# Optimization experiments

Measured on AMD Instinct MI355X. Metric: run time of the kernel, lower is better.

The kernel has to match this reference:

```python
import jax, jax.numpy as jnp
import numpy as np

B_IMG, T_PER, DIN = 8, 4096, 1176
D, E, BN, L, TOP_K, OUT = 1024, 8, 64, 4, 2, 4096


def setup_inputs() -> dict:
    key = jax.random.key(0)
    ks = jax.random.split(key, 16)
    s = 0.02
    inp = {
        "pixel_values": jax.random.normal(ks[0], (B_IMG * T_PER, DIN), jnp.float32),
        "image_grid_thw": jnp.tile(jnp.array([[1, 64, 64]], dtype=jnp.int64), (B_IMG, 1)),
        # in_proj (no bias)
        "w_in": jax.random.normal(ks[1], (DIN, D), jnp.float32) * s,
        # skin classifier: Linear(D,64) -> ReLU -> Linear(64,3)
        "w_sc1": jax.random.normal(ks[2], (D, 64), jnp.float32) * s,
        "b_sc1": jnp.zeros((64,), jnp.float32),
        "w_sc2": jax.random.normal(ks[3], (64, 3), jnp.float32) * s,
        "b_sc2": jnp.zeros((3,), jnp.float32),
        # per-adapter-layer routers (stacked over L)
        "w_rimg": jax.random.normal(ks[4], (L, D, E), jnp.float32) * s,
        "w_rskin": jax.random.normal(ks[5], (L, 3, E), jnp.float32) * s,
        # per-layer, per-expert MLP: Linear(D,BN) -> ReLU -> Linear(BN,D)
        "ew1": jax.random.normal(ks[6], (L, E, D, BN), jnp.float32) * s,
        "eb1": jnp.zeros((L, E, BN), jnp.float32),
        "ew2": jax.random.normal(ks[7], (L, E, BN, D), jnp.float32) * s,
        "eb2": jnp.zeros((L, E, D), jnp.float32),
        # out_proj
        "w_out": jax.random.normal(ks[8], (D, OUT), jnp.float32) * s,
        "b_out": jnp.zeros((OUT,), jnp.float32),
    }
    return inp


def _forward(pixel_values, image_grid_thw, w_in, w_sc1, b_sc1, w_sc2, b_sc2,
             w_rimg, w_rskin, ew1, eb1, ew2, eb2, w_out, b_out):
    B = image_grid_thw.shape[0]
    T = pixel_values.shape[0] // B  # equal chunk sizes (t*h*w identical per image)
    x = pixel_values.reshape(B, T, -1)

    def per_image(xc):  # xc: [T, din]
        h = xc @ w_in  # [T, D]
        g = h.mean(0)
        skin_logits = jax.nn.relu(g @ w_sc1 + b_sc1) @ w_sc2 + b_sc2  # [3]
        skin_probs = jax.nn.softmax(skin_logits)

        def layer(carry, params):
            h, aux = carry
            wri, wrs, W1, B1, W2, B2 = params
            logits = h @ wri + skin_probs @ wrs  # [T, E]
            probs = jax.nn.softmax(logits, axis=-1)
            tp, ti = jax.lax.top_k(probs, TOP_K)
            tp = tp / (tp.sum(-1, keepdims=True) + 1e-6)
            rows = jnp.arange(h.shape[0])[:, None]
            # dense per-token expert weights (0 for non-selected experts)
            wfull = jnp.zeros_like(probs).at[rows, ti].add(tp)
            mask = jnp.zeros_like(probs).at[rows, ti].add(1.0)
            h1 = jax.nn.relu(jnp.einsum('td,edb->teb', h, W1) + B1)  # [T,E,BN]
            h2 = jnp.einsum('teb,ebd->ted', h1, W2) + B2             # [T,E,D]
            moe_out = jnp.einsum('ted,te->td', h2, wfull)
            aux = aux + (probs.mean(0) * mask.mean(0)).sum() * probs.shape[-1]
            return (h + moe_out, aux), None

        (h, aux), _ = jax.lax.scan(layer, (h, jnp.zeros((), h.dtype)),
                                   (w_rimg, w_rskin, ew1, eb1, ew2, eb2))
        return h.mean(0), skin_logits, aux

    pooled, skin_logits, aux = jax.vmap(per_image)(x)
    vision_proj = pooled @ w_out + b_out
    return pooled, vision_proj, aux.sum(), skin_logits


def reference(pixel_values, image_grid_thw, w_in, w_sc1, b_sc1, w_sc2, b_sc2,
              w_rimg, w_rskin, ew1, eb1, ew2, eb2, w_out, b_out):
    return _forward(pixel_values, image_grid_thw, w_in, w_sc1, b_sc1, w_sc2, b_sc2,
                    w_rimg, w_rskin, ew1, eb1, ew2, eb2, w_out, b_out)
```

## Files before the change

kernel.cpp:

```cpp
#include <hip/hip_runtime.h>
#include <math.h>

#define TPI  4096
#define TT   32768
#define DIN  1176
#define KP   1216
#define DM   1024
#define NE   8
#define BN   64
#define NL   4
#define DOUT 4096
#define TBLK 32

typedef __attribute__((ext_vector_type(4))) float floatx4;
typedef __attribute__((ext_vector_type(8))) short bf16x8;
typedef unsigned int uint;

__device__ inline short f2bf(float x) {
    unsigned u = __float_as_uint(x);
    u += 0x7fffu + ((u >> 16) & 1u);
    return (short)(u >> 16);
}
__device__ inline float bf2f(short h) {
    return __uint_as_float(((unsigned)(unsigned short)h) << 16);
}

#define GLP(p) ((const __attribute__((address_space(1))) void*)(p))
#define LDSP(p) ((__attribute__((address_space(3))) void*)(p))
#define ASYNC16(g, s) __builtin_amdgcn_global_load_lds(GLP(g), LDSP(s), 16, 0, 0)

#define OFF_H0    0ul
#define OFF_H1    67108864ul
#define OFF_XB    67108864ul
#define OFF_WBT   146800640ul
#define OFF_E1T   149291008ul
#define OFF_E2T   153485312ul
#define OFF_BTOK  157679616ul
#define OFF_BW1   157810688ul
#define OFF_BW2   157941760ul
#define OFF_T2E   158072832ul
#define OFF_T2W   158203904ul
#define OFF_Z     158466048ul
#define Z_BYTES   39232ul
#define OFF_RB    158505280ul
#define OFF_WRT   158506304ul

__global__ __launch_bounds__(256) void convx_kernel(
    const float* __restrict__ X, short* __restrict__ Xb)
{
    const long row = blockIdx.x;
    const float* src = X + row * (long)DIN;
    short* dst = Xb + row * (long)KP;
    for (int i = threadIdx.x; i < 304; i += 256) {
        short4 s;
        if (i < 294) {
            float4 v = *(const float4*)(src + i * 4);
            s.x = f2bf(v.x); s.y = f2bf(v.y); s.z = f2bf(v.z); s.w = f2bf(v.w);
        } else {
            s.x = 0; s.y = 0; s.z = 0; s.w = 0;
        }
        *(short4*)(dst + i * 4) = s;
    }
}

__global__ __launch_bounds__(256) void transp_kernel(
    const float* __restrict__ src, short* __restrict__ dst, int RS, int CS, int DK)
{
    __shared__ float tb[64][65];
    const int kt = blockIdx.x * 64, nt = blockIdx.y * 64;
    const long sb = (long)blockIdx.z * RS * CS;
    const long db = (long)blockIdx.z * CS * DK;
    const int rr = threadIdx.x >> 6, cc = threadIdx.x & 63;
#pragma unroll
    for (int i = 0; i < 16; ++i) {
        int r = i * 4 + rr;
        int k = kt + r, n = nt + cc;
        tb[r][cc] = (k < RS && n < CS) ? src[sb + (long)k * CS + n] : 0.0f;
    }
    __syncthreads();
#pragma unroll
    for (int i = 0; i < 16; ++i) {
        int r = i * 4 + rr;
        int n = nt + r, k = kt + cc;
        if (n < CS && k < DK) dst[db + (long)n * DK + k] = f2bf(tb[cc][r]);
    }
}

__global__ __launch_bounds__(256) void wrt_kernel(
    const float* __restrict__ w_rimg, short* __restrict__ wrT)
{
    const int l = blockIdx.x >> 4, e = blockIdx.x & 15;
    short* dst = wrT + ((long)l * 16 + e) * 1024;
    if (e < 8) {
        const float* src = w_rimg + (long)l * 8192 + e;
        for (int k = threadIdx.x; k < 1024; k += 256) dst[k] = f2bf(src[k * 8]);
    } else {
        for (int k = threadIdx.x; k < 1024; k += 256) dst[k] = 0;
    }
}

__global__ __launch_bounds__(256) void gemm_in_mfma(
    const short* __restrict__ Xb, const short* __restrict__ Wbt,
    short* __restrict__ Hb, float* __restrict__ g)
{
    __shared__ __align__(16) short As[128 * 64];
    __shared__ __align__(16) short Bs[128 * 64];
    const int tid = threadIdx.x;
    const int m0 = blockIdx.x * 128, n0 = blockIdx.y * 128;
    const int w = tid >> 6, lane = tid & 63;
    const int quad = lane >> 4, l15 = lane & 15;
    const int wm = (w >> 1) * 64, wn = (w & 1) * 64;

    floatx4 acc[4][4];
#pragma unroll
    for (int i = 0; i < 4; ++i)
#pragma unroll
        for (int j = 0; j < 4; ++j) acc[i][j] = 0.0f;

    const int r = tid >> 3;
    const int gofs = ((tid & 7) ^ (r & 7)) * 8;
    const short* ap = Xb + (long)(m0 + r) * KP + gofs;
    const short* bp = Wbt + (long)(n0 + r) * KP + gofs;
    short* asd = As + tid * 8;
    short* bsd = Bs + tid * 8;
    const int rx = l15 & 7;

    for (int k0 = 0; k0 < KP; k0 += 64) {
        __syncthreads();
#pragma unroll
        for (int i = 0; i < 4; ++i) {
            ASYNC16(ap + (long)i * 32 * KP + k0, asd + i * 2048);
            ASYNC16(bp + (long)i * 32 * KP + k0, bsd + i * 2048);
        }
        __syncthreads();
#pragma unroll
        for (int kk = 0; kk < 2; ++kk) {
            bf16x8 af[4], bfr[4];
#pragma unroll
            for (int i = 0; i < 4; ++i)
                af[i] = *(const bf16x8*)&As[(wm + i * 16 + l15) * 64 + (((kk * 4 + quad)) ^ rx) * 8];
#pragma unroll
            for (int j = 0; j < 4; ++j)
                bfr[j] = *(const bf16x8*)&Bs[(wn + j * 16 + l15) * 64 + (((kk * 4 + quad)) ^ rx) * 8];
#pragma unroll
            for (int i = 0; i < 4; ++i)
#pragma unroll
                for (int j = 0; j < 4; ++j)
                    acc[i][j] = __builtin_amdgcn_mfma_f32_16x16x32_bf16(af[i], bfr[j], acc[i][j], 0, 0, 0);
        }
    }
    const int img = m0 >> 12;
#pragma unroll
    for (int j = 0; j < 4; ++j) {
        float cs = 0.0f;
#pragma unroll
        for (int i = 0; i < 4; ++i)
#pragma unroll
            for (int r2 = 0; r2 < 4; ++r2) {
                short hv = f2bf(acc[i][j][r2]);
                Hb[(long)(m0 + wm + i * 16 + quad * 4 + r2) * DM + n0 + wn + j * 16 + l15] =
                    hv;
                cs += bf2f(hv);
            }
        cs += __shfl_xor(cs, 16);
        cs += __shfl_xor(cs, 32);
        if (quad == 0)
            atomicAdd(&g[img * DM + n0 + wn + j * 16 + l15], cs * (1.0f / 4096.0f));
    }
}

__global__ __launch_bounds__(256) void colmean_kernel(
    const short* __restrict__ Hb, float* __restrict__ outp)
{
    const int col = blockIdx.x * 256 + threadIdx.x;
    const int img = blockIdx.y;
    const int t0 = blockIdx.z * 256;
    const short* p = Hb + ((long)img * TPI + t0) * DM + col;
    float s = 0.0f;
#pragma unroll 8
    for (int t = 0; t < 256; ++t) s += bf2f(p[(long)t * DM]);
    atomicAdd(&outp[img * DM + col], s * (1.0f / 4096.0f));
}

__global__ __launch_bounds__(256) void skin1_kernel(
    const float* __restrict__ g, const float* __restrict__ w_sc1,
    const float* __restrict__ b_sc1, float* __restrict__ hsg)
{
    __shared__ float red[4][64];
    const int img = blockIdx.x;
    const int part = threadIdx.x >> 6, c = threadIdx.x & 63;
    float s = 0.0f;
    for (int i = 0; i < 256; ++i) {
        int d = part * 256 + i;
        s += g[img * DM + d] * w_sc1[d * 64 + c];
    }
    red[part][c] = s;
    __syncthreads();
    if (part == 0) {
        float v = red[0][c] + red[1][c] + red[2][c] + red[3][c] + b_sc1[c];
        hsg[img * 64 + c] = fmaxf(v, 0.0f);
    }
}

__global__ __launch_bounds__(256) void skin2_kernel(
    const float* __restrict__ hsg, const float* __restrict__ w_sc2, const float* __restrict__ b_sc2,
    const float* __restrict__ w_rskin, float* __restrict__ skin_logits_out, float* __restrict__ rb)
{
    __shared__ float l3[24];
    __shared__ float sp[24];
    const int tid = threadIdx.x;
    if (tid < 24) {
        int img = tid / 3, j = tid % 3;
        float s = b_sc2[j];
        for (int c = 0; c < 64; ++c) s += hsg[img * 64 + c] * w_sc2[c * 3 + j];
        l3[tid] = s;
        skin_logits_out[tid] = s;
    }
    __syncthreads();
    if (tid < 8) {
        float v0 = l3[tid * 3], v1 = l3[tid * 3 + 1], v2 = l3[tid * 3 + 2];
        float m = fmaxf(v0, fmaxf(v1, v2));
        float e0 = expf(v0 - m), e1 = expf(v1 - m), e2 = expf(v2 - m);
        float inv = 1.0f / (e0 + e1 + e2);
        sp[tid * 3] = e0 * inv; sp[tid * 3 + 1] = e1 * inv; sp[tid * 3 + 2] = e2 * inv;
    }
    __syncthreads();
    {
        int l = tid >> 6, img = (tid >> 3) & 7, e = tid & 7;
        float s = 0.0f;
#pragma unroll
        for (int c = 0; c < 3; ++c) s += sp[img * 3 + c] * w_rskin[(l * 3 + c) * 8 + e];
        rb[tid] = s;
    }
}

__global__ __launch_bounds__(256) void router_kernel(
    const short* __restrict__ Hb, const short* __restrict__ wrT, const float* __restrict__ rb,
    uint* __restrict__ top2e, float* __restrict__ top2w, int* __restrict__ counts_pair,
    float* __restrict__ sum_probs, float* __restrict__ mask_cnt, int l)
{
    __shared__ __align__(16) short As[8 * 64 * 32];
    __shared__ float lgS[64 * 9];
    const int tid = threadIdx.x;
    const int tok0 = blockIdx.x * 64;
    const int img = tok0 >> 12;
    const int w = tid >> 6, lane = tid & 63;
    const int quad = lane >> 4, l15 = lane & 15;

    const short* rowptr = Hb + (long)(tok0 + w * 16 + (lane >> 2)) * DM + (lane & 3) * 8;
    short* sdst = As + tid * 8;
    const short* wrl = wrT + (long)l * 16 * 1024 + l15 * 1024 + quad * 8;

    floatx4 acc = 0.0f;
    for (int k0 = 0; k0 < DM; k0 += 256) {
        __syncthreads();
#pragma unroll
        for (int c = 0; c < 8; ++c) ASYNC16(rowptr + k0 + c * 32, sdst + c * 2048);
        __syncthreads();
#pragma unroll
        for (int c = 0; c < 8; ++c) {
            bf16x8 af = *(const bf16x8*)&As[c * 2048 + (w * 16 + l15) * 32 + quad * 8];
            bf16x8 bf = *(const bf16x8*)(wrl + k0 + c * 32);
            acc = __builtin_amdgcn_mfma_f32_16x16x32_bf16(af, bf, acc, 0, 0, 0);
        }
    }
    if (l15 < 8) {
#pragma unroll
        for (int r = 0; r < 4; ++r) lgS[(w * 16 + quad * 4 + r) * 9 + l15] = acc[r];
    }
    __syncthreads();

    if (tid < 64) {
        const int token = tok0 + tid;
        float p[8];
        float mx = -1e30f;
#pragma unroll
        for (int e = 0; e < 8; ++e) {
            float v = lgS[tid * 9 + e] + rb[l * 64 + img * 8 + e];
            p[e] = v; mx = fmaxf(mx, v);
        }
        float s = 0.0f;
#pragma unroll
        for (int e = 0; e < 8; ++e) { p[e] = expf(p[e] - mx); s += p[e]; }
        float inv = 1.0f / s;
#pragma unroll
        for (int e = 0; e < 8; ++e) p[e] *= inv;

        int i1 = 0; float b1v = p[0];
#pragma unroll
        for (int e = 1; e < 8; ++e) if (p[e] > b1v) { b1v = p[e]; i1 = e; }
        int i2 = -1; float b2v = -1.0f;
#pragma unroll
        for (int e = 0; e < 8; ++e) if (e != i1 && p[e] > b2v) { b2v = p[e]; i2 = e; }
        float den = b1v + b2v + 1e-6f;
        top2e[token] = (uint)i1 | ((uint)i2 << 8);
        top2w[2 * token] = b1v / den;
        top2w[2 * token + 1] = b2v / den;

        atomicAdd(&counts_pair[l * 64 + i1 * 8 + i2], 1);

        for (int slot = 0; slot < 2; ++slot) {
            int esel = slot ? i2 : i1;
#pragma unroll
            for (int e = 0; e < 8; ++e) {
                unsigned long long m = __ballot(esel == e);
                int pc = __popcll(m);
                if (pc && tid == (__ffsll(m) - 1))
                    atomicAdd(&mask_cnt[l * 64 + img * 8 + e], (float)pc);
            }
        }
#pragma unroll
        for (int e = 0; e < 8; ++e) {
            float rsum = p[e];
            for (int off = 32; off > 0; off >>= 1) rsum += __shfl_down(rsum, off);
            if (tid == 0) atomicAdd(&sum_probs[l * 64 + img * 8 + e], rsum);
        }
    }
}

__global__ __launch_bounds__(256) void scatter_kernel(
    const uint* __restrict__ top2e, const float* __restrict__ top2w,
    const int* __restrict__ counts_pair, int* __restrict__ cursors,
    int* __restrict__ btok, float* __restrict__ bw1, float* __restrict__ bw2, int l)
{
    __shared__ int pofS[64];
    const int tid = threadIdx.x;
    if (tid < 64) {
        int c = counts_pair[l * 64 + tid];
        int x = c;
#pragma unroll
        for (int off = 1; off < 64; off <<= 1) {
            int y = __shfl_up(x, off);
            if (tid >= off) x += y;
        }
        pofS[tid] = x - c;
    }
    __syncthreads();
    const int t = blockIdx.x * 256 + tid;
    const int lane = tid & 63;
    uint pe = top2e[t];
    int p = (int)(pe & 255u) * 8 + (int)((pe >> 8) & 255u);
    float w1 = top2w[2 * t], w2 = top2w[2 * t + 1];
    int myoff = pofS[p];
    unsigned long long rem = __ballot(true);
    while (rem) {
        int leader = __ffsll(rem) - 1;
        int pv = __shfl(p, leader);
        unsigned long long m = __ballot(p == pv);
        int basep = 0;
        if (lane == leader) basep = atomicAdd(&cursors[l * 64 + pv], __popcll(m));
        basep = __shfl(basep, leader);
        if (p == pv) {
            int pos = basep + __popcll(m & ((1ull << lane) - 1ull));
            int s = myoff + pos;
            btok[s] = t;
            bw1[s] = w1;
            bw2[s] = w2;
        }
        rem &= ~m;
    }
}

__global__ __launch_bounds__(256, 3) void expert_pair(
    const short* __restrict__ Hin, short* __restrict__ Hout,
    int* __restrict__ counts_pair,
    const int* __restrict__ btok, const float* __restrict__ bw1, const float* __restrict__ bw2,
    const short* __restrict__ ew1t, const float* __restrict__ eb1,
    const short* __restrict__ ew2t, const float* __restrict__ eb2,
    const short* __restrict__ wrT, const float* __restrict__ rb,
    uint* __restrict__ top2e, float* __restrict__ top2w,
    float* __restrict__ sum_probs, float* __restrict__ mask_cnt, int l)
{
    __shared__ __align__(16) short As[2][TBLK * 256];
    __shared__ __align__(16) short h1ab[2][TBLK * 72];
    __shared__ int tkS[TBLK];
    __shared__ float w1S[TBLK], w2S[TBLK];
    __shared__ int pofS[64], cntS[64], tpS[64];
    __shared__ int nworkS;
    __shared__ float spLDS[64], mkLDS[64];

    short* h1a = &h1ab[0][0];
    short* h1b = &h1ab[1][0];
    float* lgF = (float*)&h1ab[0][0];

    const int tid = threadIdx.x;
    const int w = tid >> 6, lane = tid & 63;
    const int quad = lane >> 4, l15 = lane & 15;

    if (tid < 64) {
        int c = counts_pair[l * 64 + tid];
        cntS[tid] = c;
        int x = c;
#pragma unroll
        for (int off = 1; off < 64; off <<= 1) {
            int y = __shfl_up(x, off);
            if (tid >= off) x += y;
        }
        pofS[tid] = x - c;
        int nb = (c + TBLK - 1) >> 5;
        int t = nb;
#pragma unroll
        for (int off = 1; off < 64; off <<= 1) {
            int y = __shfl_up(t, off);
            if (tid >= off) t += y;
        }
        tpS[tid] = t;
        if (tid == 63) nworkS = t;
    }
    __syncthreads();
    const int nwork = nworkS;

    const int bswz = (int)((blockIdx.x & 7) * (gridDim.x >> 3) + (blockIdx.x >> 3));

    const int srow0 = tid >> 5;
    const int sj = tid & 31;

    for (int wi = bswz; wi < nwork; wi += gridDim.x) {
        int p = 0;
        while (p < 63 && tpS[p] <= wi) ++p;
        const int cnt = cntS[p];
        const int nbp = (cnt + TBLK - 1) >> 5;
        const int base = (wi - (tpS[p] - nbp)) * TBLK;
        const int ea = p >> 3, eb = p & 7;
        const int off = pofS[p];
        const int lea = l * 8 + ea, leb = l * 8 + eb;

        __syncthreads();

        long srcrow[4];
#pragma unroll
        for (int cc = 0; cc < 4; ++cc) {
            const int row = cc * 8 + srow0;
            const int tokr = ((base + row) < cnt) ? btok[off + base + row] : 0;
            srcrow[cc] = (long)tokr * DM + ((sj ^ (row & 7)) << 3);
        }
        if (tid < TBLK) {
            bool valid = (base + tid) < cnt;
            int s = off + base + tid;
            tkS[tid] = valid ? btok[s] : 0;
            w1S[tid] = valid ? bw1[s] : 0.0f;
            w2S[tid] = valid ? bw2[s] : 0.0f;
        }
        if (tid < 64) { spLDS[tid] = 0.0f; mkLDS[tid] = 0.0f; }

#pragma unroll
        for (int cc = 0; cc < 4; ++cc)
            ASYNC16(Hin + srcrow[cc], &As[0][(cc * 256 + tid) * 8]);
        __syncthreads();

        floatx4 acc1a[2], acc1b[2];
#pragma unroll
        for (int i = 0; i < 2; ++i) { acc1a[i] = 0.0f; acc1b[i] = 0.0f; }
        const short* w1ap = ew1t + ((long)lea * BN + w * 16 + l15) * DM + quad * 8;
        const short* w1bp = ew1t + ((long)leb * BN + w * 16 + l15) * DM + quad * 8;

#pragma unroll
        for (int s = 0; s < 4; ++s) {
            const int nxt = (s < 3) ? (s + 1) * 256 : 0;
            short* dst = &As[(s & 1) ^ 1][0];
#pragma unroll
            for (int cc = 0; cc < 4; ++cc)
                ASYNC16(Hin + srcrow[cc] + nxt, dst + (cc * 256 + tid) * 8);
            const short* cur = &As[s & 1][0];
            const int k0 = s * 256;
#pragma unroll
            for (int c = 0; c < 8; ++c) {
                bf16x8 ba = *(const bf16x8*)(w1ap + k0 + c * 32);
                bf16x8 bb = *(const bf16x8*)(w1bp + k0 + c * 32);
#pragma unroll
                for (int i = 0; i < 2; ++i) {
                    const int tok = i * 16 + l15;
                    bf16x8 af = *(const bf16x8*)&cur[tok * 256 + (((c * 4 + quad) ^ (tok & 7)) << 3)];
                    acc1a[i] = __builtin_amdgcn_mfma_f32_16x16x32_bf16(af, ba, acc1a[i], 0, 0, 0);
                    acc1b[i] = __builtin_amdgcn_mfma_f32_16x16x32_bf16(af, bb, acc1b[i], 0, 0, 0);
                }
            }
            __syncthreads();
        }
        {
            float b1av = eb1[lea * BN + w * 16 + l15];
            float b1bv = eb1[leb * BN + w * 16 + l15];
#pragma unroll
            for (int i = 0; i < 2; ++i)
#pragma unroll
                for (int r = 0; r < 4; ++r) {
                    h1a[(i * 16 + quad * 4 + r) * 72 + w * 16 + l15] =
                        f2bf(fmaxf(acc1a[i][r] + b1av, 0.0f));
                    h1b[(i * 16 + quad * 4 + r) * 72 + w * 16 + l15] =
                        f2bf(fmaxf(acc1b[i][r] + b1bv, 0.0f));
                }
        }
        __syncthreads();

        bf16x8 hra[2][2], hrb[2][2];
#pragma unroll
        for (int kk = 0; kk < 2; ++kk)
#pragma unroll
            for (int tj = 0; tj < 2; ++tj) {
                hra[kk][tj] = *(const bf16x8*)&h1a[(tj * 16 + l15) * 72 + kk * 32 + quad * 8];
                hrb[kk][tj] = *(const bf16x8*)&h1b[(tj * 16 + l15) * 72 + kk * 32 + quad * 8];
            }

        const short* w2ap = ew2t + ((long)lea * DM + w * 16 + l15) * 64 + quad * 8;
        const short* w2bp = ew2t + ((long)leb * DM + w * 16 + l15) * 64 + quad * 8;
        const short* wrp = wrT + ((long)(l + 1 < NL ? l + 1 : 0) * 16 + l15) * 1024 + quad * 8;

        floatx4 acc_lg[2];
#pragma unroll
        for (int tf = 0; tf < 2; ++tf) acc_lg[tf] = 0.0f;

#pragma unroll
        for (int gidx = 0; gidx < 4; ++gidx) {
            const int g0 = gidx * 256;
            if (gidx < 3) {
                short* dst = &As[(gidx & 1) ^ 1][0];
#pragma unroll
                for (int cc = 0; cc < 4; ++cc)
                    ASYNC16(Hin + srcrow[cc] + (g0 + 256), dst + (cc * 256 + tid) * 8);
            }
            short* cur = &As[gidx & 1][0];
#pragma unroll
            for (int ns = 0; ns < 4; ++ns) {
                const int n0 = g0 + ns * 64;
                floatx4 a2a[2], a2b[2];
#pragma unroll
                for (int tj = 0; tj < 2; ++tj) { a2a[tj] = 0.0f; a2b[tj] = 0.0f; }
#pragma unroll
                for (int kk = 0; kk < 2; ++kk) {
                    bf16x8 wa = *(const bf16x8*)(w2ap + (long)n0 * 64 + kk * 32);
                    bf16x8 wb = *(const bf16x8*)(w2bp + (long)n0 * 64 + kk * 32);
#pragma unroll
                    for (int tj = 0; tj < 2; ++tj) {
                        a2a[tj] = __builtin_amdgcn_mfma_f32_16x16x32_bf16(wa, hra[kk][tj], a2a[tj], 0, 0, 0);
                        a2b[tj] = __builtin_amdgcn_mfma_f32_16x16x32_bf16(wb, hrb[kk][tj], a2b[tj], 0, 0, 0);
                    }
                }
                const int nloc = ns * 64 + w * 16 + quad * 4;
                const int jch = nloc >> 3, jof = nloc & 7;
                float4 b2av = *(const float4*)&eb2[lea * DM + g0 + nloc];
                float4 b2bv = *(const float4*)&eb2[leb * DM + g0 + nloc];
#pragma unroll
                for (int tj = 0; tj < 2; ++tj) {
                    int tk = tj * 16 + l15;
                    float w1v = w1S[tk], w2v = w2S[tk];
                    short* slot = &cur[tk * 256 + ((jch ^ (tk & 7)) << 3) + jof];
                    short4 res = *(short4*)slot;
                    short4 o;
                    o.x = f2bf(bf2f(res.x) + w1v * (a2a[tj][0] + b2av.x) + w2v * (a2b[tj][0] + b2bv.x));
                    o.y = f2bf(bf2f(res.y) + w1v * (a2a[tj][1] + b2av.y) + w2v * (a2b[tj][1] + b2bv.y));
                    o.z = f2bf(bf2f(res.z) + w1v * (a2a[tj][2] + b2av.z) + w2v * (a2b[tj][2] + b2bv.z));
                    o.w = f2bf(bf2f(res.w) + w1v * (a2a[tj][3] + b2av.w) + w2v * (a2b[tj][3] + b2bv.w));
                    *(short4*)slot = o;
                }
            }
            __syncthreads();

            if (l < 3) {
#pragma unroll
                for (int kk = 0; kk < 2; ++kk) {
                    const int c = w * 2 + kk;
                    bf16x8 wf = *(const bf16x8*)(wrp + g0 + c * 32);
#pragma unroll
                    for (int tf = 0; tf < 2; ++tf) {
                        const int tok = tf * 16 + l15;
                        bf16x8 of = *(const bf16x8*)&cur[tok * 256 + (((c * 4 + quad) ^ (tok & 7)) << 3)];
                        acc_lg[tf] = __builtin_amdgcn_mfma_f32_16x16x32_bf16(wf, of, acc_lg[tf], 0, 0, 0);
                    }
                }
            }
#pragma unroll
            for (int cc = 0; cc < 4; ++cc) {
                const int row = cc * 8 + srow0;
                if ((base + row) < cnt) {
                    int4 v = *(const int4*)&cur[row * 256 + ((sj ^ (row & 7)) << 3)];
                    *(int4*)(Hout + (long)tkS[row] * DM + g0 + (sj << 3)) = v;
                }
            }
            __syncthreads();
        }

        if (l < 3) {
#pragma unroll
            for (int tf = 0; tf < 2; ++tf)
                *(floatx4*)&lgF[(w * 32 + tf * 16 + l15) * 16 + quad * 4] = acc_lg[tf];
            __syncthreads();
            if (tid < TBLK) {
                const bool valid = (base + tid) < cnt;
                const int token = tkS[tid];
                const int img = token >> 12;
                float pb[8]; float mx = -1e30f;
#pragma unroll
                for (int e = 0; e < 8; ++e) {
                    float v = lgF[tid * 16 + e] + lgF[(32 + tid) * 16 + e]
                            + lgF[(64 + tid) * 16 + e] + lgF[(96 + tid) * 16 + e]
                            + rb[(l + 1) * 64 + img * 8 + e];
                    pb[e] = v; mx = fmaxf(mx, v);
                }
                float s = 0.0f;
#pragma unroll
                for (int e = 0; e < 8; ++e) { pb[e] = expf(pb[e] - mx); s += pb[e]; }
                float inv = 1.0f / s;
#pragma unroll
                for (int e = 0; e < 8; ++e) pb[e] *= inv;
                int i1 = 0; float b1v = pb[0];
#pragma unroll
                for (int e = 1; e < 8; ++e) if (pb[e] > b1v) { b1v = pb[e]; i1 = e; }
                int i2 = -1; float b2v = -1.0f;
#pragma unroll
                for (int e = 0; e < 8; ++e) if (e != i1 && pb[e] > b2v) { b2v = pb[e]; i2 = e; }
                if (valid) {
                    float den = b1v + b2v + 1e-6f;
                    top2e[token] = (uint)i1 | ((uint)i2 << 8);
                    top2w[2 * token] = b1v / den;
                    top2w[2 * token + 1] = b2v / den;
                    atomicAdd(&counts_pair[(l + 1) * 64 + i1 * 8 + i2], 1);
#pragma unroll
                    for (int e = 0; e < 8; ++e) atomicAdd(&spLDS[img * 8 + e], pb[e]);
                    atomicAdd(&mkLDS[img * 8 + i1], 1.0f);
                    atomicAdd(&mkLDS[img * 8 + i2], 1.0f);
                }
            }
            __syncthreads();
            if (tid < 64) {
                float v = spLDS[tid];
                if (v != 0.0f) atomicAdd(&sum_probs[(l + 1) * 64 + tid], v);
                float mz = mkLDS[tid];
                if (mz != 0.0f) atomicAdd(&mask_cnt[(l + 1) * 64 + tid], mz);
            }
        }
    }
}

__global__ __launch_bounds__(256) void vproj_kernel(
    const float* __restrict__ pooled, const float* __restrict__ w_out,
    const float* __restrict__ b_out, float* __restrict__ outp)
{
    __shared__ float ps[8 * 128];
    const int tid = threadIdx.x;
    const int n = blockIdx.x * 256 + tid;
    const int d0 = blockIdx.y * 128;
#pragma unroll
    for (int i = 0; i < 4; ++i) {
        int idx = tid + i * 256;
        ps[idx] = pooled[(idx >> 7) * DM + d0 + (idx & 127)];
    }
    __syncthreads();
    float acc[8];
    float binit = (blockIdx.y == 0) ? b_out[n] : 0.0f;
#pragma unroll
    for (int img = 0; img < 8; ++img) acc[img] = binit;
    for (int d = 0; d < 128; ++d) {
        float wv = w_out[(long)(d0 + d) * DOUT + n];
#pragma unroll
        for (int img = 0; img < 8; ++img) acc[img] += ps[img * 128 + d] * wv;
    }
#pragma unroll
    for (int img = 0; img < 8; ++img) atomicAdd(&outp[img * DOUT + n], acc[img]);
}

__global__ __launch_bounds__(64) void aux_kernel(
    const float* __restrict__ sum_probs, const float* __restrict__ mask_cnt,
    float* __restrict__ outp)
{
    const int tid = threadIdx.x;
    float v = 0.0f;
    if (tid < 32) {
        float s = 0.0f;
#pragma unroll
        for (int e = 0; e < 8; ++e) s += sum_probs[tid * 8 + e] * mask_cnt[tid * 8 + e];
        v = s * (8.0f / (4096.0f * 4096.0f));
    }
    for (int off = 32; off > 0; off >>= 1) v += __shfl_down(v, off);
    if (tid == 0) outp[0] = v;
}

extern "C" void kernel_launch(void* const* d_in, const int* in_sizes, int n_in,
                              void* d_out, int out_size, void* d_ws, size_t ws_size,
                              hipStream_t stream) {
    const float* X       = (const float*)d_in[0];
    const float* w_in    = (const float*)d_in[2];
    const float* w_sc1   = (const float*)d_in[3];
    const float* b_sc1   = (const float*)d_in[4];
    const float* w_sc2   = (const float*)d_in[5];
    const float* b_sc2   = (const float*)d_in[6];
    const float* w_rimg  = (const float*)d_in[7];
    const float* w_rskin = (const float*)d_in[8];
    const float* ew1     = (const float*)d_in[9];
    const float* eb1     = (const float*)d_in[10];
    const float* ew2     = (const float*)d_in[11];
    const float* eb2     = (const float*)d_in[12];
    const float* w_out   = (const float*)d_in[13];
    const float* b_out   = (const float*)d_in[14];

    float* out = (float*)d_out;
    char* ws = (char*)d_ws;

    short* H0   = (short*)(ws + OFF_H0);
    short* H1   = (short*)(ws + OFF_H1);
    short* Xb   = (short*)(ws + OFF_XB);
    short* Wbt  = (short*)(ws + OFF_WBT);
    short* ew1t = (short*)(ws + OFF_E1T);
    short* ew2t = (short*)(ws + OFF_E2T);
    int*   btok = (int*)(ws + OFF_BTOK);
    float* bw1  = (float*)(ws + OFF_BW1);
    float* bw2  = (float*)(ws + OFF_BW2);
    uint*  top2e = (uint*)(ws + OFF_T2E);
    float* top2w = (float*)(ws + OFF_T2W);
    int*   counts_pair = (int*)(ws + OFF_Z);
    int*   cursors     = (int*)(ws + OFF_Z + 1024);
    float* sum_probs   = (float*)(ws + OFF_Z + 2368);
    float* mask_cnt    = (float*)(ws + OFF_Z + 3392);
    float* g           = (float*)(ws + OFF_Z + 4416);
    float* hsg         = (float*)(ws + OFF_Z + 37184);
    float* rb          = (float*)(ws + OFF_RB);
    short* wrT         = (short*)(ws + OFF_WRT);

    hipMemsetAsync(d_out, 0, (size_t)out_size * sizeof(float), stream);
    hipMemsetAsync(ws + OFF_Z, 0, Z_BYTES, stream);

    dim3 b256(256);
    convx_kernel<<<TT, b256, 0, stream>>>(X, Xb);
    transp_kernel<<<dim3(19, 16, 1), b256, 0, stream>>>(w_in, Wbt, DIN, DM, KP);
    transp_kernel<<<dim3(16, 1, 32), b256, 0, stream>>>(ew1, ew1t, DM, BN, DM);
    transp_kernel<<<dim3(1, 16, 32), b256, 0, stream>>>(ew2, ew2t, BN, DM, BN);
    wrt_kernel<<<64, b256, 0, stream>>>(w_rimg, wrT);
    gemm_in_mfma<<<dim3(256, 8), b256, 0, stream>>>(Xb, Wbt, H0, g);
    skin1_kernel<<<8, b256, 0, stream>>>(g, w_sc1, b_sc1, hsg);
    skin2_kernel<<<1, b256, 0, stream>>>(hsg, w_sc2, b_sc2, w_rskin, out + 40961, rb);
    router_kernel<<<512, b256, 0, stream>>>(H0, wrT, rb, top2e, top2w,
                                            counts_pair, sum_probs, mask_cnt, 0);

    short* Hc = H0;
    short* Hn = H1;
    for (int l = 0; l < NL; ++l) {
        scatter_kernel<<<128, b256, 0, stream>>>(top2e, top2w, counts_pair, cursors,
                                                 btok, bw1, bw2, l);
        expert_pair<<<1152, b256, 0, stream>>>(Hc, Hn, counts_pair, btok, bw1, bw2,
                                               ew1t, eb1, ew2t, eb2, wrT, rb,
                                               top2e, top2w, sum_probs, mask_cnt, l);
        short* tmp = Hc; Hc = Hn; Hn = tmp;
    }
    colmean_kernel<<<dim3(4, 8, 16), b256, 0, stream>>>(Hc, out);
    vproj_kernel<<<dim3(16, 8), b256, 0, stream>>>(out, w_out, b_out, out + 8192);
    aux_kernel<<<1, 64, 0, stream>>>(sum_probs, mask_cnt, out + 40960);
}
```

Measured before the change: 1.510 ms.

## Double expert token tile to 64 with narrower K-chunks and register-prefetched W1

The expert_pair kernel now processes 64 tokens per work item instead of 32, staging 128-column chunks of activations and prefetching the next W1 fragments into registers while computing the current chunk. This doubles reuse of each expert weight load across tokens, at the cost of more registers and wasted rows in partially filled tiles. Separately, convx uses a grid-stride loop over fewer blocks, and gemm_in is launched as a 1D grid with a block-index swizzle for better cache locality.

```diff
diff --git a/kernel.cpp b/kernel.cpp
--- a/kernel.cpp
+++ b/kernel.cpp
@@ -10,7 +10,7 @@
 #define BN   64
 #define NL   4
 #define DOUT 4096
-#define TBLK 32
+#define TBLK 64
 
 typedef __attribute__((ext_vector_type(4))) float floatx4;
 typedef __attribute__((ext_vector_type(8))) short bf16x8;
@@ -48,18 +48,19 @@
 __global__ __launch_bounds__(256) void convx_kernel(
     const float* __restrict__ X, short* __restrict__ Xb)
 {
-    const long row = blockIdx.x;
-    const float* src = X + row * (long)DIN;
-    short* dst = Xb + row * (long)KP;
-    for (int i = threadIdx.x; i < 304; i += 256) {
-        short4 s;
-        if (i < 294) {
-            float4 v = *(const float4*)(src + i * 4);
-            s.x = f2bf(v.x); s.y = f2bf(v.y); s.z = f2bf(v.z); s.w = f2bf(v.w);
-        } else {
-            s.x = 0; s.y = 0; s.z = 0; s.w = 0;
-        }
-        *(short4*)(dst + i * 4) = s;
+    for (long row = blockIdx.x; row < TT; row += gridDim.x) {
+        const float* src = X + row * (long)DIN;
+        short* dst = Xb + row * (long)KP;
+        for (int i = threadIdx.x; i < 304; i += 256) {
+            short4 s;
+            if (i < 294) {
+                float4 v = *(const float4*)(src + i * 4);
+                s.x = f2bf(v.x); s.y = f2bf(v.y); s.z = f2bf(v.z); s.w = f2bf(v.w);
+            } else {
+                s.x = 0; s.y = 0; s.z = 0; s.w = 0;
+            }
+            *(short4*)(dst + i * 4) = s;
+        }
     }
 }
 
@@ -106,7 +107,9 @@
     __shared__ __align__(16) short As[128 * 64];
     __shared__ __align__(16) short Bs[128 * 64];
     const int tid = threadIdx.x;
-    const int m0 = blockIdx.x * 128, n0 = blockIdx.y * 128;
+    const int bid = blockIdx.x;
+    const int swz = (bid & 7) * 256 + (bid >> 3);
+    const int m0 = (swz & 255) * 128, n0 = (swz >> 8) * 128;
     const int w = tid >> 6, lane = tid & 63;
     const int quad = lane >> 4, l15 = lane & 15;
     const int wm = (w >> 1) * 64, wn = (w & 1) * 64;
@@ -371,7 +374,7 @@
     uint* __restrict__ top2e, float* __restrict__ top2w,
     float* __restrict__ sum_probs, float* __restrict__ mask_cnt, int l)
 {
-    __shared__ __align__(16) short As[2][TBLK * 256];
+    __shared__ __align__(16) short As[2][TBLK * 128];
     __shared__ __align__(16) short h1ab[2][TBLK * 72];
     __shared__ int tkS[TBLK];
     __shared__ float w1S[TBLK], w2S[TBLK];
@@ -386,6 +389,7 @@
     const int tid = threadIdx.x;
     const int w = tid >> 6, lane = tid & 63;
     const int quad = lane >> 4, l15 = lane & 15;
+    const int rx = l15 & 7;
 
     if (tid < 64) {
         int c = counts_pair[l * 64 + tid];
@@ -397,7 +401,7 @@
             if (tid >= off) x += y;
         }
         pofS[tid] = x - c;
-        int nb = (c + TBLK - 1) >> 5;
+        int nb = (c + 63) >> 6;
         int t = nb;
 #pragma unroll
         for (int off = 1; off < 64; off <<= 1) {
@@ -412,14 +416,14 @@
 
     const int bswz = (int)((blockIdx.x & 7) * (gridDim.x >> 3) + (blockIdx.x >> 3));
 
-    const int srow0 = tid >> 5;
-    const int sj = tid & 31;
+    const int srow = tid >> 4;
+    const int chp  = tid & 15;
 
     for (int wi = bswz; wi < nwork; wi += gridDim.x) {
         int p = 0;
         while (p < 63 && tpS[p] <= wi) ++p;
         const int cnt = cntS[p];
-        const int nbp = (cnt + TBLK - 1) >> 5;
+        const int nbp = (cnt + 63) >> 6;
         const int base = (wi - (tpS[p] - nbp)) * TBLK;
         const int ea = p >> 3, eb = p & 7;
         const int off = pofS[p];
@@ -430,9 +434,9 @@
         long srcrow[4];
 #pragma unroll
         for (int cc = 0; cc < 4; ++cc) {
-            const int row = cc * 8 + srow0;
+            const int row = cc * 16 + srow;
             const int tokr = ((base + row) < cnt) ? btok[off + base + row] : 0;
-            srcrow[cc] = (long)tokr * DM + ((sj ^ (row & 7)) << 3);
+            srcrow[cc] = (long)tokr * DM + ((chp ^ (row & 7)) << 3);
         }
         if (tid < TBLK) {
             bool valid = (base + tid) < cnt;
@@ -440,63 +444,79 @@
             tkS[tid] = valid ? btok[s] : 0;
             w1S[tid] = valid ? bw1[s] : 0.0f;
             w2S[tid] = valid ? bw2[s] : 0.0f;
-        }
-        if (tid < 64) { spLDS[tid] = 0.0f; mkLDS[tid] = 0.0f; }
+            spLDS[tid] = 0.0f;
+            mkLDS[tid] = 0.0f;
+        }
 
 #pragma unroll
         for (int cc = 0; cc < 4; ++cc)
             ASYNC16(Hin + srcrow[cc], &As[0][(cc * 256 + tid) * 8]);
-        __syncthreads();
-
-        floatx4 acc1a[2], acc1b[2];
-#pragma unroll
-        for (int i = 0; i < 2; ++i) { acc1a[i] = 0.0f; acc1b[i] = 0.0f; }
         const short* w1ap = ew1t + ((long)lea * BN + w * 16 + l15) * DM + quad * 8;
         const short* w1bp = ew1t + ((long)leb * BN + w * 16 + l15) * DM + quad * 8;
-
-#pragma unroll
-        for (int s = 0; s < 4; ++s) {
-            const int nxt = (s < 3) ? (s + 1) * 256 : 0;
-            short* dst = &As[(s & 1) ^ 1][0];
+        bf16x8 wCa[4], wCb[4];
+#pragma unroll
+        for (int c = 0; c < 4; ++c) {
+            wCa[c] = *(const bf16x8*)(w1ap + c * 32);
+            wCb[c] = *(const bf16x8*)(w1bp + c * 32);
+        }
+        __syncthreads();
+
+        floatx4 acc1a[4], acc1b[4];
+#pragma unroll
+        for (int i = 0; i < 4; ++i) { acc1a[i] = 0.0f; acc1b[i] = 0.0f; }
+
+#pragma unroll
+        for (int r = 0; r < 8; ++r) {
+            const int nofs = (r < 7) ? (r + 1) * 128 : 0;
+            short* dst = &As[(r & 1) ^ 1][0];
 #pragma unroll
             for (int cc = 0; cc < 4; ++cc)
-                ASYNC16(Hin + srcrow[cc] + nxt, dst + (cc * 256 + tid) * 8);
-            const short* cur = &As[s & 1][0];
-            const int k0 = s * 256;
-#pragma unroll
-            for (int c = 0; c < 8; ++c) {
-                bf16x8 ba = *(const bf16x8*)(w1ap + k0 + c * 32);
-                bf16x8 bb = *(const bf16x8*)(w1bp + k0 + c * 32);
-#pragma unroll
-                for (int i = 0; i < 2; ++i) {
-                    const int tok = i * 16 + l15;
-                    bf16x8 af = *(const bf16x8*)&cur[tok * 256 + (((c * 4 + quad) ^ (tok & 7)) << 3)];
-                    acc1a[i] = __builtin_amdgcn_mfma_f32_16x16x32_bf16(af, ba, acc1a[i], 0, 0, 0);
-                    acc1b[i] = __builtin_amdgcn_mfma_f32_16x16x32_bf16(af, bb, acc1b[i], 0, 0, 0);
+                ASYNC16(Hin + srcrow[cc] + nofs, dst + (cc * 256 + tid) * 8);
+            bf16x8 wNa[4], wNb[4];
+            if (r < 7) {
+#pragma unroll
+                for (int c = 0; c < 4; ++c) {
+                    wNa[c] = *(const bf16x8*)(w1ap + (r + 1) * 128 + c * 32);
+                    wNb[c] = *(const bf16x8*)(w1bp + (r + 1) * 128 + c * 32);
+                }
+            }
+            const short* cur = &As[r & 1][0];
+#pragma unroll
+            for (int c = 0; c < 4; ++c) {
+                const int cpos = (((c * 4 + quad) ^ rx) << 3);
+#pragma unroll
+                for (int i = 0; i < 4; ++i) {
+                    bf16x8 af = *(const bf16x8*)&cur[(i * 16 + l15) * 128 + cpos];
+                    acc1a[i] = __builtin_amdgcn_mfma_f32_16x16x32_bf16(af, wCa[c], acc1a[i], 0, 0, 0);
+                    acc1b[i] = __builtin_amdgcn_mfma_f32_16x16x32_bf16(af, wCb[c], acc1b[i], 0, 0, 0);
                 }
             }
             __syncthreads();
+            if (r < 7) {
+#pragma unroll
+                for (int c = 0; c < 4; ++c) { wCa[c] = wNa[c]; wCb[c] = wNb[c]; }
+            }
         }
         {
             float b1av = eb1[lea * BN + w * 16 + l15];
             float b1bv = eb1[leb * BN + w * 16 + l15];
 #pragma unroll
-            for (int i = 0; i < 2; ++i)
-#pragma unroll
-                for (int r = 0; r < 4; ++r) {
-                    h1a[(i * 16 + quad * 4 + r) * 72 + w * 16 + l15] =
-                        f2bf(fmaxf(acc1a[i][r] + b1av, 0.0f));
-                    h1b[(i * 16 + quad * 4 + r) * 72 + w * 16 + l15] =
-                        f2bf(fmaxf(acc1b[i][r] + b1bv, 0.0f));
+            for (int i = 0; i < 4; ++i)
+#pragma unroll
+                for (int r2 = 0; r2 < 4; ++r2) {
+                    h1a[(i * 16 + quad * 4 + r2) * 72 + w * 16 + l15] =
+                        f2bf(fmaxf(acc1a[i][r2] + b1av, 0.0f));
+                    h1b[(i * 16 + quad * 4 + r2) * 72 + w * 16 + l15] =
+                        f2bf(fmaxf(acc1b[i][r2] + b1bv, 0.0f));
                 }
         }
         __syncthreads();
 
-        bf16x8 hra[2][2], hrb[2][2];
+        bf16x8 hra[2][4], hrb[2][4];
 #pragma unroll
         for (int kk = 0; kk < 2; ++kk)
 #pragma unroll
-            for (int tj = 0; tj < 2; ++tj) {
+            for (int tj = 0; tj < 4; ++tj) {
                 hra[kk][tj] = *(const bf16x8*)&h1a[(tj * 16 + l15) * 72 + kk * 32 + quad * 8];
                 hrb[kk][tj] = *(const bf16x8*)&h1b[(tj * 16 + l15) * 72 + kk * 32 + quad * 8];
             }
@@ -505,32 +525,32 @@
         const short* w2bp = ew2t + ((long)leb * DM + w * 16 + l15) * 64 + quad * 8;
         const short* wrp = wrT + ((long)(l + 1 < NL ? l + 1 : 0) * 16 + l15) * 1024 + quad * 8;
 
-        floatx4 acc_lg[2];
-#pragma unroll
-        for (int tf = 0; tf < 2; ++tf) acc_lg[tf] = 0.0f;
-
-#pragma unroll
-        for (int gidx = 0; gidx < 4; ++gidx) {
-            const int g0 = gidx * 256;
-            if (gidx < 3) {
-                short* dst = &As[(gidx & 1) ^ 1][0];
+        floatx4 acc_lg[4];
+#pragma unroll
+        for (int tf = 0; tf < 4; ++tf) acc_lg[tf] = 0.0f;
+
+#pragma unroll
+        for (int gi = 0; gi < 8; ++gi) {
+            const int g0 = gi * 128;
+            if (gi < 7) {
+                short* dst = &As[(gi & 1) ^ 1][0];
 #pragma unroll
                 for (int cc = 0; cc < 4; ++cc)
-                    ASYNC16(Hin + srcrow[cc] + (g0 + 256), dst + (cc * 256 + tid) * 8);
-            }
-            short* cur = &As[gidx & 1][0];
-#pragma unroll
-            for (int ns = 0; ns < 4; ++ns) {
+                    ASYNC16(Hin + srcrow[cc] + (g0 + 128), dst + (cc * 256 + tid) * 8);
+            }
+            short* cur = &As[gi & 1][0];
+#pragma unroll
+            for (int ns = 0; ns < 2; ++ns) {
                 const int n0 = g0 + ns * 64;
-                floatx4 a2a[2], a2b[2];
-#pragma unroll
-                for (int tj = 0; tj < 2; ++tj) { a2a[tj] = 0.0f; a2b[tj] = 0.0f; }
+                floatx4 a2a[4], a2b[4];
+#pragma unroll
+                for (int tj = 0; tj < 4; ++tj) { a2a[tj] = 0.0f; a2b[tj] = 0.0f; }
 #pragma unroll
                 for (int kk = 0; kk < 2; ++kk) {
                     bf16x8 wa = *(const bf16x8*)(w2ap + (long)n0 * 64 + kk * 32);
                     bf16x8 wb = *(const bf16x8*)(w2bp + (long)n0 * 64 + kk * 32);
 #pragma unroll
-                    for (int tj = 0; tj < 2; ++tj) {
+                    for (int tj = 0; tj < 4; ++tj) {
                         a2a[tj] = __builtin_amdgcn_mfma_f32_16x16x32_bf16(wa, hra[kk][tj], a2a[tj], 0, 0, 0);
                         a2b[tj] = __builtin_amdgcn_mfma_f32_16x16x32_bf16(wb, hrb[kk][tj], a2b[tj], 0, 0, 0);
                     }
@@ -540,10 +560,10 @@
                 float4 b2av = *(const float4*)&eb2[lea * DM + g0 + nloc];
                 float4 b2bv = *(const float4*)&eb2[leb * DM + g0 + nloc];
 #pragma unroll
-                for (int tj = 0; tj < 2; ++tj) {
+                for (int tj = 0; tj < 4; ++tj) {
                     int tk = tj * 16 + l15;
                     float w1v = w1S[tk], w2v = w2S[tk];
-                    short* slot = &cur[tk * 256 + ((jch ^ (tk & 7)) << 3) + jof];
+                    short* slot = &cur[tk * 128 + ((jch ^ (tk & 7)) << 3) + jof];
                     short4 res = *(short4*)slot;
                     short4 o;
                     o.x = f2bf(bf2f(res.x) + w1v * (a2a[tj][0] + b2av.x) + w2v * (a2b[tj][0] + b2bv.x));
@@ -556,24 +576,20 @@
             __syncthreads();
 
             if (l < 3) {
-#pragma unroll
-                for (int kk = 0; kk < 2; ++kk) {
-                    const int c = w * 2 + kk;
-                    bf16x8 wf = *(const bf16x8*)(wrp + g0 + c * 32);
-#pragma unroll
-                    for (int tf = 0; tf < 2; ++tf) {
-                        const int tok = tf * 16 + l15;
-                        bf16x8 of = *(const bf16x8*)&cur[tok * 256 + (((c * 4 + quad) ^ (tok & 7)) << 3)];
-                        acc_lg[tf] = __builtin_amdgcn_mfma_f32_16x16x32_bf16(wf, of, acc_lg[tf], 0, 0, 0);
-                    }
+                bf16x8 wf = *(const bf16x8*)(wrp + g0 + w * 32);
+                const int cpos = (((w * 4 + quad) ^ rx) << 3);
+#pragma unroll
+                for (int tf = 0; tf < 4; ++tf) {
+                    bf16x8 of = *(const bf16x8*)&cur[(tf * 16 + l15) * 128 + cpos];
+                    acc_lg[tf] = __builtin_amdgcn_mfma_f32_16x16x32_bf16(wf, of, acc_lg[tf], 0, 0, 0);
                 }
             }
 #pragma unroll
             for (int cc = 0; cc < 4; ++cc) {
-                const int row = cc * 8 + srow0;
+                const int row = cc * 16 + srow;
                 if ((base + row) < cnt) {
-                    int4 v = *(const int4*)&cur[row * 256 + ((sj ^ (row & 7)) << 3)];
-                    *(int4*)(Hout + (long)tkS[row] * DM + g0 + (sj << 3)) = v;
+                    int4 v = *(const int4*)&cur[row * 128 + ((chp ^ (row & 7)) << 3)];
+                    *(int4*)(Hout + (long)tkS[row] * DM + g0 + (chp << 3)) = v;
                 }
             }
             __syncthreads();
@@ -581,8 +597,8 @@
 
         if (l < 3) {
 #pragma unroll
-            for (int tf = 0; tf < 2; ++tf)
-                *(floatx4*)&lgF[(w * 32 + tf * 16 + l15) * 16 + quad * 4] = acc_lg[tf];
+            for (int tf = 0; tf < 4; ++tf)
+                *(floatx4*)&lgF[(w * 64 + tf * 16 + l15) * 16 + quad * 4] = acc_lg[tf];
             __syncthreads();
             if (tid < TBLK) {
                 const bool valid = (base + tid) < cnt;
@@ -591,8 +607,8 @@
                 float pb[8]; float mx = -1e30f;
 #pragma unroll
                 for (int e = 0; e < 8; ++e) {
-                    float v = lgF[tid * 16 + e] + lgF[(32 + tid) * 16 + e]
-                            + lgF[(64 + tid) * 16 + e] + lgF[(96 + tid) * 16 + e]
+                    float v = lgF[tid * 16 + e] + lgF[(64 + tid) * 16 + e]
+                            + lgF[(128 + tid) * 16 + e] + lgF[(192 + tid) * 16 + e]
                             + rb[(l + 1) * 64 + img * 8 + e];
                     pb[e] = v; mx = fmaxf(mx, v);
                 }
@@ -719,12 +735,12 @@
     hipMemsetAsync(ws + OFF_Z, 0, Z_BYTES, stream);
 
     dim3 b256(256);
-    convx_kernel<<<TT, b256, 0, stream>>>(X, Xb);
+    convx_kernel<<<2048, b256, 0, stream>>>(X, Xb);
     transp_kernel<<<dim3(19, 16, 1), b256, 0, stream>>>(w_in, Wbt, DIN, DM, KP);
     transp_kernel<<<dim3(16, 1, 32), b256, 0, stream>>>(ew1, ew1t, DM, BN, DM);
     transp_kernel<<<dim3(1, 16, 32), b256, 0, stream>>>(ew2, ew2t, BN, DM, BN);
     wrt_kernel<<<64, b256, 0, stream>>>(w_rimg, wrT);
-    gemm_in_mfma<<<dim3(256, 8), b256, 0, stream>>>(Xb, Wbt, H0, g);
+    gemm_in_mfma<<<2048, b256, 0, stream>>>(Xb, Wbt, H0, g);
     skin1_kernel<<<8, b256, 0, stream>>>(g, w_sc1, b_sc1, hsg);
     skin2_kernel<<<1, b256, 0, stream>>>(hsg, w_sc2, b_sc2, w_rskin, out + 40961, rb);
     router_kernel<<<512, b256, 0, stream>>>(H0, wrT, rb, top2e, top2w,
@@ -735,9 +751,9 @@
     for (int l = 0; l < NL; ++l) {
         scatter_kernel<<<128, b256, 0, stream>>>(top2e, top2w, counts_pair, cursors,
                                                  btok, bw1, bw2, l);
-        expert_pair<<<1152, b256, 0, stream>>>(Hc, Hn, counts_pair, btok, bw1, bw2,
-                                               ew1t, eb1, ew2t, eb2, wrT, rb,
-                                               top2e, top2w, sum_probs, mask_cnt, l);
+        expert_pair<<<576, b256, 0, stream>>>(Hc, Hn, counts_pair, btok, bw1, bw2,
+                                              ew1t, eb1, ew2t, eb2, wrT, rb,
+                                              top2e, top2w, sum_probs, mask_cnt, l);
         short* tmp = Hc; Hc = Hn; Hn = tmp;
     }
     colmean_kernel<<<dim3(4, 8, 16), b256, 0, stream>>>(Hc, out);
```

Result: no change. 1.512 ms (+0.1%).
